# Optimization experiments

Hardware: AMD Instinct MI355X
Metric: run time of the kernel (lower is better)

Reference implementation:

```python
import jax, jax.numpy as jnp
import numpy as np

NEG_INF = -1e9

def setup_inputs() -> dict:
    key = jax.random.key(0)
    k1, k2, k3, k4, k5 = jax.random.split(key, 5)
    N, F_IN, F_OUT, H = 8192, 128, 32, 4
    node_features = jax.random.normal(k1, (N, F_IN), dtype=jnp.float32)
    adj_matrix = jax.random.randint(k2, (N, N), 0, 2, dtype=jnp.int32)
    # stacked per-head params (original: one Linear W [F_IN,F_OUT] + attention vec a [2*F_OUT] per head)
    W = jax.random.normal(k3, (H, F_IN, F_OUT), dtype=jnp.float32) * (1.0 / np.sqrt(F_IN))
    a_src = jax.random.normal(k4, (H, F_OUT), dtype=jnp.float32) * 0.1
    a_dst = jax.random.normal(k5, (H, F_OUT), dtype=jnp.float32) * 0.1
    return {"node_features": node_features, "adj_matrix": adj_matrix,
            "W": W, "a_src": a_src, "a_dst": a_dst}

def reference(node_features, adj_matrix, W, a_src, a_dst):
    alpha = 0.2  # LeakyReLU negative slope
    # project: [H, N, F_OUT]
    h = jnp.einsum('nf,hfo->hno', node_features, W)
    # GAT scores e_ij = LeakyReLU(a_src . h_i + a_dst . h_j), shape [H, N, N]
    e_src = jnp.einsum('hno,ho->hn', h, a_src)  # [H, N]
    e_dst = jnp.einsum('hno,ho->hn', h, a_dst)  # [H, N]
    e = jax.nn.leaky_relu(e_src[:, :, None] + e_dst[:, None, :], negative_slope=alpha)
    mask = (adj_matrix > 0)[None, :, :]
    attn = jax.nn.softmax(jnp.where(mask, e, NEG_INF), axis=-1)  # [H, N, N]
    out = jnp.einsum('hij,hjo->hio', attn, h)  # [H, N, F_OUT]
    # concat heads along feature dim -> [N, H*F_OUT]
    H_, N_, O_ = out.shape
    return jnp.transpose(out, (1, 0, 2)).reshape(N_, H_ * O_)
```

## Files before the change

### kernel.cpp

```cpp
#include <hip/hip_runtime.h>
#include <hip/hip_bf16.h>

#define NTOT 8192
#define FIN 128
#define FOUT 32
#define NH 4
#define NSEG 4
#define SEGJ (NTOT / NSEG)

typedef __attribute__((ext_vector_type(4))) float f32x4;
typedef __attribute__((ext_vector_type(4))) int i32x4;
typedef __attribute__((ext_vector_type(4))) unsigned int u32x4;
typedef __attribute__((ext_vector_type(8))) __bf16 bf16x8;
typedef unsigned long long u64;
typedef unsigned int u32;

__device__ __forceinline__ unsigned short f2bf(float x) {
  __hip_bfloat16 h = __float2bfloat16(x);
  return *reinterpret_cast<unsigned short*>(&h);
}

__global__ __launch_bounds__(256, 2) void k1_project(
    const float* __restrict__ X, const float* __restrict__ W,
    float* __restrict__ h, unsigned short* __restrict__ panel) {
  __shared__ float Xs[32 * 128];
  __shared__ float Ws[32 * 128];
  __shared__ unsigned short Hs[128 * 40];
  int t = threadIdx.x;
  int nb = blockIdx.x * 32;

  const f32x4* Xg = reinterpret_cast<const f32x4*>(X + (size_t)nb * FIN);
  f32x4* Xs4 = reinterpret_cast<f32x4*>(Xs);
#pragma unroll
  for (int r = 0; r < 4; ++r) Xs4[t + r * 256] = Xg[t + r * 256];

  int ng = t >> 5, oq = t & 31;
  int n0 = ng * 4, o0 = oq * 4;
  f32x4 acc[4];
#pragma unroll
  for (int nn = 0; nn < 4; ++nn) acc[nn] = (f32x4){0.f, 0.f, 0.f, 0.f};

  for (int kp = 0; kp < 4; ++kp) {
    __syncthreads();
#pragma unroll
    for (int r = 0; r < 4; ++r) {
      int q = t + r * 256;
      int flat = q * 4;
      int kk = flat >> 7;
      int c = flat & 127;
      int hdd = c >> 5;
      int oo = c & 31;
      *reinterpret_cast<f32x4*>(&Ws[kk * 128 + c]) =
          *reinterpret_cast<const f32x4*>(W + hdd * (FIN * FOUT) +
                                          (kp * 32 + kk) * FOUT + oo);
    }
    __syncthreads();
#pragma unroll 8
    for (int kk = 0; kk < 32; ++kk) {
      f32x4 wv = *reinterpret_cast<const f32x4*>(&Ws[kk * 128 + o0]);
#pragma unroll
      for (int nn = 0; nn < 4; ++nn)
        acc[nn] += Xs[(n0 + nn) * 128 + kp * 32 + kk] * wv;
    }
  }
#pragma unroll
  for (int nn = 0; nn < 4; ++nn) {
    *reinterpret_cast<f32x4*>(&h[(size_t)(nb + n0 + nn) * 128 + o0]) = acc[nn];
#pragma unroll
    for (int c = 0; c < 4; ++c)
      Hs[(o0 + c) * 40 + (n0 + nn)] = f2bf(acc[nn][c]);
  }
  __syncthreads();
  int jt = blockIdx.x;
#pragma unroll
  for (int it = 0; it < 2; ++it) {
    int item = t + it * 256;
    int p = item >> 6;
    int l = item & 63;
    int o = p * 16 + (l & 15);
    u32x4 v = *reinterpret_cast<const u32x4*>(&Hs[o * 40 + (l >> 4) * 8]);
    *reinterpret_cast<u32x4*>(panel + (size_t)(p * 256 + jt) * 512 + l * 8) = v;
  }
}

__global__ __launch_bounds__(256, 2) void k2_scores(
    const float* __restrict__ h, const float* __restrict__ a_src,
    const float* __restrict__ a_dst, float* __restrict__ Sf,
    float* __restrict__ E1f, float* __restrict__ E2f,
    unsigned short* __restrict__ Dbf, unsigned short* __restrict__ F1bf,
    unsigned short* __restrict__ F2bf) {
  int n = blockIdx.x * 256 + threadIdx.x;
  const f32x4* hv = reinterpret_cast<const f32x4*>(h + (size_t)n * 128);
  const f32x4* as4 = reinterpret_cast<const f32x4*>(a_src);
  const f32x4* ad4 = reinterpret_cast<const f32x4*>(a_dst);
  int jm = n >> 6, jo = n & 63;
#pragma unroll
  for (int hd = 0; hd < NH; ++hd) {
    f32x4 sa = {0.f, 0.f, 0.f, 0.f}, da = {0.f, 0.f, 0.f, 0.f};
#pragma unroll
    for (int q = 0; q < 8; ++q) {
      f32x4 x = hv[hd * 8 + q];
      sa += x * as4[hd * 8 + q];
      da += x * ad4[hd * 8 + q];
    }
    float s = (sa[0] + sa[1]) + (sa[2] + sa[3]);
    float d = (da[0] + da[1]) + (da[2] + da[3]);
    Sf[hd * NTOT + n] = s;
    E1f[hd * NTOT + n] = expf(s);
    E2f[hd * NTOT + n] = expf(0.2f * s);
    int ti = (jm * 4 + hd) * 64 + jo;
    Dbf[ti] = f2bf(d);
    F1bf[ti] = f2bf(expf(d));
    F2bf[ti] = f2bf(expf(0.2f * d));
  }
}

__global__ __launch_bounds__(256)
__attribute__((amdgpu_waves_per_eu(2))) void k3_attn(
    const int* __restrict__ adj, const float* __restrict__ Sf,
    const float* __restrict__ E1f, const float* __restrict__ E2f,
    const unsigned short* __restrict__ Dbf,
    const unsigned short* __restrict__ F1bf,
    const unsigned short* __restrict__ F2bf,
    const unsigned short* __restrict__ panel, float* __restrict__ pacc,
    float* __restrict__ plsum) {
  const int N = NTOT;
  int tid = threadIdx.x;
  int w = tid >> 6, l = tid & 63;
  int rh = w & 1, hp = w >> 1;
  int itile = blockIdx.x >> 2, seg = blockIdx.x & 3;
  int ibase = itile * 32 + rh * 16;
  int m = l & 15, g = l >> 4, jc = g * 8;
  int row = ibase + m;
  int hd0 = hp * 2;

  float sv0 = Sf[hd0 * N + row];
  float sv1 = Sf[(hd0 + 1) * N + row];

  const int* adjr = adj + (size_t)row * N + seg * SEGJ + jc;
  const char* dB =
      (const char*)Dbf + (size_t)(seg * 32) * 512 + hd0 * 128 + jc * 2;
  const char* f1B =
      (const char*)F1bf + (size_t)(seg * 32) * 512 + hd0 * 128 + jc * 2;
  const char* f2B =
      (const char*)F2bf + (size_t)(seg * 32) * 512 + hd0 * 128 + jc * 2;
  const char* pB = (const char*)panel +
                   ((size_t)(hd0 * 2) * 256 + seg * 64) * 1024 + (size_t)l * 16;
  const size_t PS = (size_t)256 * 1024;

  f32x4 z4 = {0.f, 0.f, 0.f, 0.f};
  f32x4 aP0[2] = {z4, z4}, aP1[2] = {z4, z4}, aPs[2] = {z4, z4};
  f32x4 aN0[2] = {z4, z4}, aN1[2] = {z4, z4}, aNs[2] = {z4, z4};
  bf16x8 bones;
  {
    u32 pat = (m == 0) ? 0x3f803f80u : 0u;
    u32x4 tmp = {pat, pat, pat, pat};
    bones = *reinterpret_cast<bf16x8*>(&tmp);
  }

#define MFM(AF, B, ACC) \
  ACC = __builtin_amdgcn_mfma_f32_16x16x32_bf16(AF, B, ACC, 0, 0, 0);

#define AFPLANE(HH, MK, Dv, F1v, F2v, B0, B1, SV)                         \
  {                                                                       \
    u32x4 aPw, aNw;                                                       \
    _Pragma("unroll") for (int p = 0; p < 4; ++p) {                       \
      float de = __uint_as_float(Dv[p] << 16);                            \
      float dodd = __uint_as_float(Dv[p] & 0xFFFF0000u);                  \
      u32 n0 = (u32)(__float_as_int((SV) + de) >> 31);                    \
      u32 n1 = (u32)(__float_as_int((SV) + dodd) >> 31);                  \
      u32 mn = __builtin_amdgcn_perm(n1, n0, 0x05040100u);                \
      aPw[p] = F1v[p] & ((MK)[p] & ~mn);                                  \
      aNw[p] = F2v[p] & ((MK)[p] & mn);                                   \
    }                                                                     \
    bf16x8 afP = *reinterpret_cast<bf16x8*>(&aPw);                        \
    bf16x8 afN = *reinterpret_cast<bf16x8*>(&aNw);                        \
    MFM(afP, B0, aP0[HH]) MFM(afP, B1, aP1[HH]) MFM(afP, bones, aPs[HH])  \
    MFM(afN, B0, aN0[HH]) MFM(afN, B1, aN1[HH]) MFM(afN, bones, aNs[HH])  \
  }

#pragma unroll 1
  for (int t = 0; t < 32; ++t) {
    const int* a_ = adjr + t * 64;
    i32x4 a0 = *reinterpret_cast<const i32x4*>(a_);
    i32x4 a1 = *reinterpret_cast<const i32x4*>(a_ + 4);
    i32x4 a2 = *reinterpret_cast<const i32x4*>(a_ + 32);
    i32x4 a3 = *reinterpret_cast<const i32x4*>(a_ + 36);
    u32x4 mkA, mkB;
#pragma unroll
    for (int p = 0; p < 2; ++p) {
      mkA[p] = __builtin_amdgcn_perm((u32)(-a0[2 * p + 1]), (u32)(-a0[2 * p]),
                                     0x05040100u);
      mkA[p + 2] = __builtin_amdgcn_perm((u32)(-a1[2 * p + 1]),
                                         (u32)(-a1[2 * p]), 0x05040100u);
      mkB[p] = __builtin_amdgcn_perm((u32)(-a2[2 * p + 1]), (u32)(-a2[2 * p]),
                                     0x05040100u);
      mkB[p + 2] = __builtin_amdgcn_perm((u32)(-a3[2 * p + 1]),
                                         (u32)(-a3[2 * p]), 0x05040100u);
    }
    size_t tb = (size_t)t * 512;
    size_t pb = (size_t)t * 2048;
#pragma unroll
    for (int hh = 0; hh < 2; ++hh) {
      float sv_ = hh ? sv1 : sv0;
      const char* d_ = dB + tb + hh * 128;
      const char* f1_ = f1B + tb + hh * 128;
      const char* f2_ = f2B + tb + hh * 128;
      const char* p0_ = pB + pb + (size_t)(hh * 2) * PS;
      const char* p1_ = p0_ + PS;
      {
        u32x4 Dv = *(const u32x4*)(d_);
        u32x4 F1v = *(const u32x4*)(f1_);
        u32x4 F2v = *(const u32x4*)(f2_);
        bf16x8 B0 = *(const bf16x8*)(p0_);
        bf16x8 B1 = *(const bf16x8*)(p1_);
        AFPLANE(hh, mkA, Dv, F1v, F2v, B0, B1, sv_)
      }
      {
        u32x4 Dv = *(const u32x4*)(d_ + 64);
        u32x4 F1v = *(const u32x4*)(f1_ + 64);
        u32x4 F2v = *(const u32x4*)(f2_ + 64);
        bf16x8 B0 = *(const bf16x8*)(p0_ + 1024);
        bf16x8 B1 = *(const bf16x8*)(p1_ + 1024);
        AFPLANE(hh, mkB, Dv, F1v, F2v, B0, B1, sv_)
      }
    }
  }
#undef AFPLANE
#undef MFM

#pragma unroll
  for (int hh = 0; hh < 2; ++hh) {
    int hd = hd0 + hh;
    int rb = ibase + g * 4;
#pragma unroll
    for (int r = 0; r < 4; ++r) {
      int rowr = rb + r;
      float e1 = E1f[hd * N + rowr], e2 = E2f[hd * N + rowr];
      if (m == 0)
        plsum[(seg * NH + hd) * N + rowr] =
            e1 * aPs[hh][r] + e2 * aNs[hh][r];
      pacc[((size_t)seg * N + rowr) * 128 + hd * 32 + m] =
          e1 * aP0[hh][r] + e2 * aN0[hh][r];
      pacc[((size_t)seg * N + rowr) * 128 + hd * 32 + 16 + m] =
          e1 * aP1[hh][r] + e2 * aN1[hh][r];
    }
  }
}

__global__ __launch_bounds__(256, 2) void k4_combine(
    const float* __restrict__ pacc, const float* __restrict__ plsum,
    float* __restrict__ out) {
  int idx = blockIdx.x * 256 + threadIdx.x;
  int i = idx >> 7;
  int c = idx & 127;
  int hd = c >> 5;
  float a = 0.f, ls = 0.f;
#pragma unroll
  for (int s = 0; s < NSEG; ++s) {
    a += pacc[((size_t)s * NTOT + i) * 128 + c];
    ls += plsum[(s * NH + hd) * NTOT + i];
  }
  out[idx] = (ls > 0.f) ? a / ls : 0.f;
}

extern "C" void kernel_launch(void* const* d_in, const int* in_sizes, int n_in,
                              void* d_out, int out_size, void* d_ws,
                              size_t ws_size, hipStream_t stream) {
  const float* X = (const float*)d_in[0];
  const int* adj = (const int*)d_in[1];
  const float* W = (const float*)d_in[2];
  const float* a_src = (const float*)d_in[3];
  const float* a_dst = (const float*)d_in[4];
  float* out = (float*)d_out;

  char* ws = (char*)d_ws;
  float* h = (float*)(ws + 0x0);
  unsigned short* panel = (unsigned short*)(ws + 0x400000);
  float* Sf = (float*)(ws + 0x600000);
  float* E1f = (float*)(ws + 0x620000);
  float* E2f = (float*)(ws + 0x640000);
  unsigned short* Dbf = (unsigned short*)(ws + 0x660000);
  unsigned short* F1bf = (unsigned short*)(ws + 0x670000);
  unsigned short* F2bf = (unsigned short*)(ws + 0x680000);
  float* pacc = (float*)(ws + 0x700000);
  float* plsum = (float*)(ws + 0x1700000);

  k1_project<<<dim3(256), dim3(256), 0, stream>>>(X, W, h, panel);
  k2_scores<<<dim3(32), dim3(256), 0, stream>>>(h, a_src, a_dst, Sf, E1f, E2f,
                                                Dbf, F1bf, F2bf);
  k3_attn<<<dim3(256 * NSEG), dim3(256), 0, stream>>>(
      adj, Sf, E1f, E2f, Dbf, F1bf, F2bf, panel, pacc, plsum);
  k4_combine<<<dim3(4096), dim3(256), 0, stream>>>(pacc, plsum, out);
}
```

Before: 170.4 us.

## Halve j-segments and software-pipeline adjacency loads with sched barriers

Reduces the column split from four to two segments, so each block processes 64 j-tiles and the grid halves. The attention loop is restructured so adjacency loads for tile t+2 are issued ahead in double-buffered registers, with sched_barrier fences fixing the order of loads and MFMA compute. The goal is to hide the latency of the large adjacency stream and cut partial-sum traffic in the combine step. In exchange there are fewer blocks for occupancy, higher register pressure, and a clamped redundant prefetch at the loop end.

```diff
diff --git a/kernel.cpp b/kernel.cpp
--- a/kernel.cpp
+++ b/kernel.cpp
@@ -5,7 +5,7 @@
 #define FIN 128
 #define FOUT 32
 #define NH 4
-#define NSEG 4
+#define NSEG 2
 #define SEGJ (NTOT / NSEG)
 
 typedef __attribute__((ext_vector_type(4))) float f32x4;
@@ -128,7 +128,7 @@
   int tid = threadIdx.x;
   int w = tid >> 6, l = tid & 63;
   int rh = w & 1, hp = w >> 1;
-  int itile = blockIdx.x >> 2, seg = blockIdx.x & 3;
+  int itile = blockIdx.x >> 1, seg = blockIdx.x & 1;
   int ibase = itile * 32 + rh * 16;
   int m = l & 15, g = l >> 4, jc = g * 8;
   int row = ibase + m;
@@ -139,13 +139,14 @@
 
   const int* adjr = adj + (size_t)row * N + seg * SEGJ + jc;
   const char* dB =
-      (const char*)Dbf + (size_t)(seg * 32) * 512 + hd0 * 128 + jc * 2;
+      (const char*)Dbf + (size_t)(seg * 64) * 512 + hd0 * 128 + jc * 2;
   const char* f1B =
-      (const char*)F1bf + (size_t)(seg * 32) * 512 + hd0 * 128 + jc * 2;
+      (const char*)F1bf + (size_t)(seg * 64) * 512 + hd0 * 128 + jc * 2;
   const char* f2B =
-      (const char*)F2bf + (size_t)(seg * 32) * 512 + hd0 * 128 + jc * 2;
+      (const char*)F2bf + (size_t)(seg * 64) * 512 + hd0 * 128 + jc * 2;
   const char* pB = (const char*)panel +
-                   ((size_t)(hd0 * 2) * 256 + seg * 64) * 1024 + (size_t)l * 16;
+                   ((size_t)(hd0 * 2) * 256 + seg * 128) * 1024 +
+                   (size_t)l * 16;
   const size_t PS = (size_t)256 * 1024;
 
   f32x4 z4 = {0.f, 0.f, 0.f, 0.f};
@@ -156,6 +157,71 @@
     u32 pat = (m == 0) ? 0x3f803f80u : 0u;
     u32x4 tmp = {pat, pat, pat, pat};
     bones = *reinterpret_cast<bf16x8*>(&tmp);
+  }
+
+  i32x4 Aa0, Aa1, Aa2, Aa3, Ba0, Ba1, Ba2, Ba3;
+  u32x4 D0a, D0b, D1a, D1b;
+  u32x4 F10a, F10b, F11a, F11b, F20a, F20b, F21a, F21b;
+  bf16x8 P00a, P00b, P01a, P01b, P10a, P10b, P11a, P11b;
+  u32x4 mkA, mkB;
+
+#define AISS(P, t_)                                            \
+  {                                                            \
+    int tc_ = (t_) > 63 ? 63 : (t_);                           \
+    const int* a_ = adjr + tc_ * 64;                           \
+    P##a0 = *reinterpret_cast<const i32x4*>(a_);               \
+    P##a1 = *reinterpret_cast<const i32x4*>(a_ + 4);           \
+    P##a2 = *reinterpret_cast<const i32x4*>(a_ + 32);          \
+    P##a3 = *reinterpret_cast<const i32x4*>(a_ + 36);          \
+  }                                                            \
+  __builtin_amdgcn_sched_barrier(0);
+
+#define TLOAD(t_)                                              \
+  {                                                            \
+    size_t tb_ = (size_t)(t_)*512;                             \
+    size_t pb_ = (size_t)(t_)*2048;                            \
+    D0a = *(const u32x4*)(dB + tb_);                           \
+    D0b = *(const u32x4*)(dB + tb_ + 64);                      \
+    D1a = *(const u32x4*)(dB + tb_ + 128);                     \
+    D1b = *(const u32x4*)(dB + tb_ + 192);                     \
+    F10a = *(const u32x4*)(f1B + tb_);                         \
+    F10b = *(const u32x4*)(f1B + tb_ + 64);                    \
+    F11a = *(const u32x4*)(f1B + tb_ + 128);                   \
+    F11b = *(const u32x4*)(f1B + tb_ + 192);                   \
+    F20a = *(const u32x4*)(f2B + tb_);                         \
+    F20b = *(const u32x4*)(f2B + tb_ + 64);                    \
+    F21a = *(const u32x4*)(f2B + tb_ + 128);                   \
+    F21b = *(const u32x4*)(f2B + tb_ + 192);                   \
+    const char* pp_ = pB + pb_;                                \
+    P00a = *(const bf16x8*)(pp_);                              \
+    P00b = *(const bf16x8*)(pp_ + 1024);                       \
+    P01a = *(const bf16x8*)(pp_ + PS);                         \
+    P01b = *(const bf16x8*)(pp_ + PS + 1024);                  \
+    P10a = *(const bf16x8*)(pp_ + 2 * PS);                     \
+    P10b = *(const bf16x8*)(pp_ + 2 * PS + 1024);              \
+    P11a = *(const bf16x8*)(pp_ + 3 * PS);                     \
+    P11b = *(const bf16x8*)(pp_ + 3 * PS + 1024);              \
+  }                                                            \
+  __builtin_amdgcn_sched_barrier(0);
+
+#define MASKS(P)                                                          \
+  {                                                                       \
+    mkA[0] = __builtin_amdgcn_perm((u32)(-P##a0[1]), (u32)(-P##a0[0]),    \
+                                   0x05040100u);                          \
+    mkA[1] = __builtin_amdgcn_perm((u32)(-P##a0[3]), (u32)(-P##a0[2]),    \
+                                   0x05040100u);                          \
+    mkA[2] = __builtin_amdgcn_perm((u32)(-P##a1[1]), (u32)(-P##a1[0]),    \
+                                   0x05040100u);                          \
+    mkA[3] = __builtin_amdgcn_perm((u32)(-P##a1[3]), (u32)(-P##a1[2]),    \
+                                   0x05040100u);                          \
+    mkB[0] = __builtin_amdgcn_perm((u32)(-P##a2[1]), (u32)(-P##a2[0]),    \
+                                   0x05040100u);                          \
+    mkB[1] = __builtin_amdgcn_perm((u32)(-P##a2[3]), (u32)(-P##a2[2]),    \
+                                   0x05040100u);                          \
+    mkB[2] = __builtin_amdgcn_perm((u32)(-P##a3[1]), (u32)(-P##a3[0]),    \
+                                   0x05040100u);                          \
+    mkB[3] = __builtin_amdgcn_perm((u32)(-P##a3[3]), (u32)(-P##a3[2]),    \
+                                   0x05040100u);                          \
   }
 
 #define MFM(AF, B, ACC) \
@@ -179,55 +245,31 @@
     MFM(afN, B0, aN0[HH]) MFM(afN, B1, aN1[HH]) MFM(afN, bones, aNs[HH])  \
   }
 
+#define COMPUTE                                            \
+  AFPLANE(0, mkA, D0a, F10a, F20a, P00a, P01a, sv0)        \
+  AFPLANE(0, mkB, D0b, F10b, F20b, P00b, P01b, sv0)        \
+  AFPLANE(1, mkA, D1a, F11a, F21a, P10a, P11a, sv1)        \
+  AFPLANE(1, mkB, D1b, F11b, F21b, P10b, P11b, sv1)
+
+  AISS(A, 0)
+  AISS(B, 1)
 #pragma unroll 1
-  for (int t = 0; t < 32; ++t) {
-    const int* a_ = adjr + t * 64;
-    i32x4 a0 = *reinterpret_cast<const i32x4*>(a_);
-    i32x4 a1 = *reinterpret_cast<const i32x4*>(a_ + 4);
-    i32x4 a2 = *reinterpret_cast<const i32x4*>(a_ + 32);
-    i32x4 a3 = *reinterpret_cast<const i32x4*>(a_ + 36);
-    u32x4 mkA, mkB;
-#pragma unroll
-    for (int p = 0; p < 2; ++p) {
-      mkA[p] = __builtin_amdgcn_perm((u32)(-a0[2 * p + 1]), (u32)(-a0[2 * p]),
-                                     0x05040100u);
-      mkA[p + 2] = __builtin_amdgcn_perm((u32)(-a1[2 * p + 1]),
-                                         (u32)(-a1[2 * p]), 0x05040100u);
-      mkB[p] = __builtin_amdgcn_perm((u32)(-a2[2 * p + 1]), (u32)(-a2[2 * p]),
-                                     0x05040100u);
-      mkB[p + 2] = __builtin_amdgcn_perm((u32)(-a3[2 * p + 1]),
-                                         (u32)(-a3[2 * p]), 0x05040100u);
-    }
-    size_t tb = (size_t)t * 512;
-    size_t pb = (size_t)t * 2048;
-#pragma unroll
-    for (int hh = 0; hh < 2; ++hh) {
-      float sv_ = hh ? sv1 : sv0;
-      const char* d_ = dB + tb + hh * 128;
-      const char* f1_ = f1B + tb + hh * 128;
-      const char* f2_ = f2B + tb + hh * 128;
-      const char* p0_ = pB + pb + (size_t)(hh * 2) * PS;
-      const char* p1_ = p0_ + PS;
-      {
-        u32x4 Dv = *(const u32x4*)(d_);
-        u32x4 F1v = *(const u32x4*)(f1_);
-        u32x4 F2v = *(const u32x4*)(f2_);
-        bf16x8 B0 = *(const bf16x8*)(p0_);
-        bf16x8 B1 = *(const bf16x8*)(p1_);
-        AFPLANE(hh, mkA, Dv, F1v, F2v, B0, B1, sv_)
-      }
-      {
-        u32x4 Dv = *(const u32x4*)(d_ + 64);
-        u32x4 F1v = *(const u32x4*)(f1_ + 64);
-        u32x4 F2v = *(const u32x4*)(f2_ + 64);
-        bf16x8 B0 = *(const bf16x8*)(p0_ + 1024);
-        bf16x8 B1 = *(const bf16x8*)(p1_ + 1024);
-        AFPLANE(hh, mkB, Dv, F1v, F2v, B0, B1, sv_)
-      }
-    }
-  }
+  for (int tt = 0; tt < 32; ++tt) {
+    TLOAD(2 * tt)
+    MASKS(A)
+    AISS(A, 2 * tt + 2)
+    COMPUTE
+    TLOAD(2 * tt + 1)
+    MASKS(B)
+    AISS(B, 2 * tt + 3)
+    COMPUTE
+  }
+#undef AISS
+#undef TLOAD
+#undef MASKS
+#undef MFM
 #undef AFPLANE
-#undef MFM
+#undef COMPUTE
 
 #pragma unroll
   for (int hh = 0; hh < 2; ++hh) {
@@ -238,8 +280,7 @@
       int rowr = rb + r;
       float e1 = E1f[hd * N + rowr], e2 = E2f[hd * N + rowr];
       if (m == 0)
-        plsum[(seg * NH + hd) * N + rowr] =
-            e1 * aPs[hh][r] + e2 * aNs[hh][r];
+        plsum[(seg * NH + hd) * N + rowr] = e1 * aPs[hh][r] + e2 * aNs[hh][r];
       pacc[((size_t)seg * N + rowr) * 128 + hd * 32 + m] =
           e1 * aP0[hh][r] + e2 * aN0[hh][r];
       pacc[((size_t)seg * N + rowr) * 128 + hd * 32 + 16 + m] =
```

Measured after the change: 171.3 us. Within noise of the previous version (+0.5%).

## Process two row groups per wave and stage column score vectors in LDS

Applied to the files above, without the earlier changes.

Each wave in the attention kernel now handles 32 rows (two 16-row groups) instead of 16, so every loaded panel B fragment and column-score vector feeds twice as many MFMAs. The per-segment D/F1/F2 bf16 tables are first copied into 48 KB of shared memory, and the inner loop reads them from there instead of from global memory. The grid is halved to match. In exchange, accumulator registers double (24 f32x4 per lane), which adds register pressure and may reduce occupancy, and the 48 KB LDS allocation per block also limits how many blocks fit on a CU.

```diff
diff --git a/kernel.cpp b/kernel.cpp
--- a/kernel.cpp
+++ b/kernel.cpp
@@ -125,32 +125,45 @@
     const unsigned short* __restrict__ panel, float* __restrict__ pacc,
     float* __restrict__ plsum) {
   const int N = NTOT;
+  __shared__ char lds[49152];
   int tid = threadIdx.x;
   int w = tid >> 6, l = tid & 63;
   int rh = w & 1, hp = w >> 1;
   int itile = blockIdx.x >> 2, seg = blockIdx.x & 3;
-  int ibase = itile * 32 + rh * 16;
+  int rowblock = itile * 64 + rh * 32;
   int m = l & 15, g = l >> 4, jc = g * 8;
-  int row = ibase + m;
   int hd0 = hp * 2;
 
-  float sv0 = Sf[hd0 * N + row];
-  float sv1 = Sf[(hd0 + 1) * N + row];
-
-  const int* adjr = adj + (size_t)row * N + seg * SEGJ + jc;
-  const char* dB =
-      (const char*)Dbf + (size_t)(seg * 32) * 512 + hd0 * 128 + jc * 2;
-  const char* f1B =
-      (const char*)F1bf + (size_t)(seg * 32) * 512 + hd0 * 128 + jc * 2;
-  const char* f2B =
-      (const char*)F2bf + (size_t)(seg * 32) * 512 + hd0 * 128 + jc * 2;
-  const char* pB = (const char*)panel +
-                   ((size_t)(hd0 * 2) * 256 + seg * 64) * 1024 + (size_t)l * 16;
-  const size_t PS = (size_t)256 * 1024;
+  {
+    const char* gD = (const char*)Dbf + (size_t)seg * 16384;
+    const char* gF1 = (const char*)F1bf + (size_t)seg * 16384;
+    const char* gF2 = (const char*)F2bf + (size_t)seg * 16384;
+#pragma unroll
+    for (int it = 0; it < 4; ++it) {
+      int off = it * 4096 + tid * 16;
+      *(u32x4*)&lds[off] = *(const u32x4*)(gD + off);
+      *(u32x4*)&lds[16384 + off] = *(const u32x4*)(gF1 + off);
+      *(u32x4*)&lds[32768 + off] = *(const u32x4*)(gF2 + off);
+    }
+  }
+  __syncthreads();
+
+  float sv[2][2];
+#pragma unroll
+  for (int hh = 0; hh < 2; ++hh)
+#pragma unroll
+    for (int rg = 0; rg < 2; ++rg)
+      sv[hh][rg] = Sf[(hd0 + hh) * N + rowblock + rg * 16 + m];
+
+  const int* adjr0 = adj + (size_t)(rowblock + m) * N + seg * SEGJ + jc;
+  const int* adjr1 = adjr0 + (size_t)16 * N;
+  const char* panB = (const char*)panel + (size_t)l * 16;
 
   f32x4 z4 = {0.f, 0.f, 0.f, 0.f};
-  f32x4 aP0[2] = {z4, z4}, aP1[2] = {z4, z4}, aPs[2] = {z4, z4};
-  f32x4 aN0[2] = {z4, z4}, aN1[2] = {z4, z4}, aNs[2] = {z4, z4};
+  f32x4 aP0[4] = {z4, z4, z4, z4}, aP1[4] = {z4, z4, z4, z4},
+        aPs[4] = {z4, z4, z4, z4};
+  f32x4 aN0[4] = {z4, z4, z4, z4}, aN1[4] = {z4, z4, z4, z4},
+        aNs[4] = {z4, z4, z4, z4};
   bf16x8 bones;
   {
     u32 pat = (m == 0) ? 0x3f803f80u : 0u;
@@ -161,68 +174,70 @@
 #define MFM(AF, B, ACC) \
   ACC = __builtin_amdgcn_mfma_f32_16x16x32_bf16(AF, B, ACC, 0, 0, 0);
 
-#define AFPLANE(HH, MK, Dv, F1v, F2v, B0, B1, SV)                         \
+#define AFPLANE(IX, MK, Dv, F1v, F2v, B0, B1, SV)                         \
   {                                                                       \
     u32x4 aPw, aNw;                                                       \
     _Pragma("unroll") for (int p = 0; p < 4; ++p) {                       \
-      float de = __uint_as_float(Dv[p] << 16);                            \
-      float dodd = __uint_as_float(Dv[p] & 0xFFFF0000u);                  \
+      float de = __uint_as_float((Dv)[p] << 16);                          \
+      float dodd = __uint_as_float((Dv)[p] & 0xFFFF0000u);                \
       u32 n0 = (u32)(__float_as_int((SV) + de) >> 31);                    \
       u32 n1 = (u32)(__float_as_int((SV) + dodd) >> 31);                  \
       u32 mn = __builtin_amdgcn_perm(n1, n0, 0x05040100u);                \
-      aPw[p] = F1v[p] & ((MK)[p] & ~mn);                                  \
-      aNw[p] = F2v[p] & ((MK)[p] & mn);                                   \
+      aPw[p] = (F1v)[p] & ((MK)[p] & ~mn);                                \
+      aNw[p] = (F2v)[p] & ((MK)[p] & mn);                                 \
     }                                                                     \
     bf16x8 afP = *reinterpret_cast<bf16x8*>(&aPw);                        \
     bf16x8 afN = *reinterpret_cast<bf16x8*>(&aNw);                        \
-    MFM(afP, B0, aP0[HH]) MFM(afP, B1, aP1[HH]) MFM(afP, bones, aPs[HH])  \
-    MFM(afN, B0, aN0[HH]) MFM(afN, B1, aN1[HH]) MFM(afN, bones, aNs[HH])  \
+    MFM(afP, B0, aP0[IX]) MFM(afP, B1, aP1[IX]) MFM(afP, bones, aPs[IX])  \
+    MFM(afN, B0, aN0[IX]) MFM(afN, B1, aN1[IX]) MFM(afN, bones, aNs[IX])  \
   }
 
 #pragma unroll 1
   for (int t = 0; t < 32; ++t) {
-    const int* a_ = adjr + t * 64;
-    i32x4 a0 = *reinterpret_cast<const i32x4*>(a_);
-    i32x4 a1 = *reinterpret_cast<const i32x4*>(a_ + 4);
-    i32x4 a2 = *reinterpret_cast<const i32x4*>(a_ + 32);
-    i32x4 a3 = *reinterpret_cast<const i32x4*>(a_ + 36);
-    u32x4 mkA, mkB;
-#pragma unroll
-    for (int p = 0; p < 2; ++p) {
-      mkA[p] = __builtin_amdgcn_perm((u32)(-a0[2 * p + 1]), (u32)(-a0[2 * p]),
-                                     0x05040100u);
-      mkA[p + 2] = __builtin_amdgcn_perm((u32)(-a1[2 * p + 1]),
-                                         (u32)(-a1[2 * p]), 0x05040100u);
-      mkB[p] = __builtin_amdgcn_perm((u32)(-a2[2 * p + 1]), (u32)(-a2[2 * p]),
-                                     0x05040100u);
-      mkB[p + 2] = __builtin_amdgcn_perm((u32)(-a3[2 * p + 1]),
-                                         (u32)(-a3[2 * p]), 0x05040100u);
-    }
-    size_t tb = (size_t)t * 512;
-    size_t pb = (size_t)t * 2048;
+    const int* a0_ = adjr0 + t * 64;
+    const int* a1_ = adjr1 + t * 64;
+    i32x4 r0A0 = *(const i32x4*)(a0_), r0A1 = *(const i32x4*)(a0_ + 4);
+    i32x4 r0B0 = *(const i32x4*)(a0_ + 32), r0B1 = *(const i32x4*)(a0_ + 36);
+    i32x4 r1A0 = *(const i32x4*)(a1_), r1A1 = *(const i32x4*)(a1_ + 4);
+    i32x4 r1B0 = *(const i32x4*)(a1_ + 32), r1B1 = *(const i32x4*)(a1_ + 36);
+    u32x4 mk[2][2];
+#define MKB(DST, A0, A1)                                                    \
+  DST[0] = __builtin_amdgcn_perm((u32)(-(A0)[1]), (u32)(-(A0)[0]),          \
+                                 0x05040100u);                              \
+  DST[1] = __builtin_amdgcn_perm((u32)(-(A0)[3]), (u32)(-(A0)[2]),          \
+                                 0x05040100u);                              \
+  DST[2] = __builtin_amdgcn_perm((u32)(-(A1)[1]), (u32)(-(A1)[0]),          \
+                                 0x05040100u);                              \
+  DST[3] = __builtin_amdgcn_perm((u32)(-(A1)[3]), (u32)(-(A1)[2]),          \
+                                 0x05040100u);
+    MKB(mk[0][0], r0A0, r0A1)
+    MKB(mk[0][1], r0B0, r0B1)
+    MKB(mk[1][0], r1A0, r1A1)
+    MKB(mk[1][1], r1B0, r1B1)
+#undef MKB
+
 #pragma unroll
     for (int hh = 0; hh < 2; ++hh) {
-      float sv_ = hh ? sv1 : sv0;
-      const char* d_ = dB + tb + hh * 128;
-      const char* f1_ = f1B + tb + hh * 128;
-      const char* f2_ = f2B + tb + hh * 128;
-      const char* p0_ = pB + pb + (size_t)(hh * 2) * PS;
-      const char* p1_ = p0_ + PS;
-      {
-        u32x4 Dv = *(const u32x4*)(d_);
-        u32x4 F1v = *(const u32x4*)(f1_);
-        u32x4 F2v = *(const u32x4*)(f2_);
-        bf16x8 B0 = *(const bf16x8*)(p0_);
-        bf16x8 B1 = *(const bf16x8*)(p1_);
-        AFPLANE(hh, mkA, Dv, F1v, F2v, B0, B1, sv_)
-      }
-      {
-        u32x4 Dv = *(const u32x4*)(d_ + 64);
-        u32x4 F1v = *(const u32x4*)(f1_ + 64);
-        u32x4 F2v = *(const u32x4*)(f2_ + 64);
-        bf16x8 B0 = *(const bf16x8*)(p0_ + 1024);
-        bf16x8 B1 = *(const bf16x8*)(p1_ + 1024);
-        AFPLANE(hh, mkB, Dv, F1v, F2v, B0, B1, sv_)
+      int hd = hd0 + hh;
+      int tb = t * 512 + hd * 128 + g * 16;
+      u32x4 DvA = *(const u32x4*)&lds[tb];
+      u32x4 DvB = *(const u32x4*)&lds[tb + 64];
+      u32x4 F1A = *(const u32x4*)&lds[16384 + tb];
+      u32x4 F1B = *(const u32x4*)&lds[16384 + tb + 64];
+      u32x4 F2A = *(const u32x4*)&lds[32768 + tb];
+      u32x4 F2B = *(const u32x4*)&lds[32768 + tb + 64];
+      size_t jtg = (size_t)(seg * 64 + t * 2);
+      const char* p0 = panB + ((size_t)(hd * 2) * 256 + jtg) * 1024;
+      const char* p1 = panB + ((size_t)(hd * 2 + 1) * 256 + jtg) * 1024;
+      bf16x8 B0A = *(const bf16x8*)(p0);
+      bf16x8 B0B = *(const bf16x8*)(p0 + 1024);
+      bf16x8 B1A = *(const bf16x8*)(p1);
+      bf16x8 B1B = *(const bf16x8*)(p1 + 1024);
+#pragma unroll
+      for (int rg = 0; rg < 2; ++rg) {
+        float sv_ = sv[hh][rg];
+        AFPLANE(hh * 2 + rg, mk[rg][0], DvA, F1A, F2A, B0A, B1A, sv_)
+        AFPLANE(hh * 2 + rg, mk[rg][1], DvB, F1B, F2B, B0B, B1B, sv_)
       }
     }
   }
@@ -231,19 +246,23 @@
 
 #pragma unroll
   for (int hh = 0; hh < 2; ++hh) {
-    int hd = hd0 + hh;
-    int rb = ibase + g * 4;
-#pragma unroll
-    for (int r = 0; r < 4; ++r) {
-      int rowr = rb + r;
-      float e1 = E1f[hd * N + rowr], e2 = E2f[hd * N + rowr];
-      if (m == 0)
-        plsum[(seg * NH + hd) * N + rowr] =
-            e1 * aPs[hh][r] + e2 * aNs[hh][r];
-      pacc[((size_t)seg * N + rowr) * 128 + hd * 32 + m] =
-          e1 * aP0[hh][r] + e2 * aN0[hh][r];
-      pacc[((size_t)seg * N + rowr) * 128 + hd * 32 + 16 + m] =
-          e1 * aP1[hh][r] + e2 * aN1[hh][r];
+#pragma unroll
+    for (int rg = 0; rg < 2; ++rg) {
+      int hd = hd0 + hh;
+      int ix = hh * 2 + rg;
+      int rb = rowblock + rg * 16 + g * 4;
+#pragma unroll
+      for (int r = 0; r < 4; ++r) {
+        int rowr = rb + r;
+        float e1 = E1f[hd * N + rowr], e2 = E2f[hd * N + rowr];
+        if (m == 0)
+          plsum[(seg * NH + hd) * N + rowr] =
+              e1 * aPs[ix][r] + e2 * aNs[ix][r];
+        pacc[((size_t)seg * N + rowr) * 128 + hd * 32 + m] =
+            e1 * aP0[ix][r] + e2 * aN0[ix][r];
+        pacc[((size_t)seg * N + rowr) * 128 + hd * 32 + 16 + m] =
+            e1 * aP1[ix][r] + e2 * aN1[ix][r];
+      }
     }
   }
 }
@@ -289,7 +308,7 @@
   k1_project<<<dim3(256), dim3(256), 0, stream>>>(X, W, h, panel);
   k2_scores<<<dim3(32), dim3(256), 0, stream>>>(h, a_src, a_dst, Sf, E1f, E2f,
                                                 Dbf, F1bf, F2bf);
-  k3_attn<<<dim3(256 * NSEG), dim3(256), 0, stream>>>(
+  k3_attn<<<dim3(128 * NSEG), dim3(256), 0, stream>>>(
       adj, Sf, E1f, E2f, Dbf, F1bf, F2bf, panel, pacc, plsum);
   k4_combine<<<dim3(4096), dim3(256), 0, stream>>>(pacc, plsum, out);
 }
```

Result: slower. 191.4 us (+12.3%).

## Prepack adjacency into bitmasks and stage panel/score tables through LDS via DMA

Applied to the files above, without the earlier changes.

A new pre-kernel compresses the int32 adjacency matrix into 64-bit ballot bitmasks stored transposed, so the attention kernel reads bits instead of full ints, and each adjacency row is then read from memory once rather than once per head pair. The score tables (D, exp(d), exp(0.2d)) are interleaved into one buffer. Panel and table tiles are double-buffered into shared memory with global_load_lds, and the grid is remapped so that each block covers 64 rows and one head pair. The cost is an extra full pass over the 256 MB adjacency in k0, plus per-iteration barriers in the main loop.

```diff
diff --git a/kernel.cpp b/kernel.cpp
--- a/kernel.cpp
+++ b/kernel.cpp
@@ -18,6 +18,26 @@
 __device__ __forceinline__ unsigned short f2bf(float x) {
   __hip_bfloat16 h = __float2bfloat16(x);
   return *reinterpret_cast<unsigned short*>(&h);
+}
+
+__device__ __forceinline__ void dma16(const void* g, void* l) {
+  __builtin_amdgcn_global_load_lds(
+      (const __attribute__((address_space(1))) void*)g,
+      (__attribute__((address_space(3))) void*)l, 16, 0, 0);
+}
+
+__global__ __launch_bounds__(256, 2) void k0_pack(
+    const int* __restrict__ adj, u64* __restrict__ bits64T) {
+  int row = blockIdx.x * 4 + (threadIdx.x >> 6);
+  int l = threadIdx.x & 63;
+  const int* ap = adj + (size_t)row * NTOT + l;
+  u64* bp = bits64T + row;
+#pragma unroll 4
+  for (int j64 = 0; j64 < NTOT / 64; ++j64) {
+    int v = ap[j64 * 64];
+    u64 mske = __ballot(v != 0);
+    if (l == 0) bp[(size_t)j64 * NTOT] = mske;
+  }
 }
 
 __global__ __launch_bounds__(256, 2) void k1_project(
@@ -87,8 +107,7 @@
     const float* __restrict__ h, const float* __restrict__ a_src,
     const float* __restrict__ a_dst, float* __restrict__ Sf,
     float* __restrict__ E1f, float* __restrict__ E2f,
-    unsigned short* __restrict__ Dbf, unsigned short* __restrict__ F1bf,
-    unsigned short* __restrict__ F2bf) {
+    unsigned short* __restrict__ Tt) {
   int n = blockIdx.x * 256 + threadIdx.x;
   const f32x4* hv = reinterpret_cast<const f32x4*>(h + (size_t)n * 128);
   const f32x4* as4 = reinterpret_cast<const f32x4*>(a_src);
@@ -108,45 +127,41 @@
     Sf[hd * NTOT + n] = s;
     E1f[hd * NTOT + n] = expf(s);
     E2f[hd * NTOT + n] = expf(0.2f * s);
-    int ti = (jm * 4 + hd) * 64 + jo;
-    Dbf[ti] = f2bf(d);
-    F1bf[ti] = f2bf(expf(d));
-    F2bf[ti] = f2bf(expf(0.2f * d));
+    int ti = jm * 1024 + hd * 192 + jo;
+    Tt[ti] = f2bf(d);
+    Tt[ti + 64] = f2bf(expf(d));
+    Tt[ti + 128] = f2bf(expf(0.2f * d));
   }
 }
 
 __global__ __launch_bounds__(256)
 __attribute__((amdgpu_waves_per_eu(2))) void k3_attn(
-    const int* __restrict__ adj, const float* __restrict__ Sf,
+    const u64* __restrict__ bits64T, const float* __restrict__ Sf,
     const float* __restrict__ E1f, const float* __restrict__ E2f,
-    const unsigned short* __restrict__ Dbf,
-    const unsigned short* __restrict__ F1bf,
-    const unsigned short* __restrict__ F2bf,
+    const unsigned short* __restrict__ Tt,
     const unsigned short* __restrict__ panel, float* __restrict__ pacc,
     float* __restrict__ plsum) {
   const int N = NTOT;
+  __shared__ char panelS[2][8192];
+  __shared__ char tabS[2][2048];
   int tid = threadIdx.x;
   int w = tid >> 6, l = tid & 63;
-  int rh = w & 1, hp = w >> 1;
-  int itile = blockIdx.x >> 2, seg = blockIdx.x & 3;
-  int ibase = itile * 32 + rh * 16;
+  int bx = blockIdx.x;
+  int itile = bx >> 3, hp = (bx >> 2) & 1, seg = bx & 3;
+  int ibase = itile * 64;
   int m = l & 15, g = l >> 4, jc = g * 8;
-  int row = ibase + m;
+  int rowbase = ibase + w * 16;
+  int row = rowbase + m;
   int hd0 = hp * 2;
+  int jm0 = seg * 32;
 
   float sv0 = Sf[hd0 * N + row];
   float sv1 = Sf[(hd0 + 1) * N + row];
 
-  const int* adjr = adj + (size_t)row * N + seg * SEGJ + jc;
-  const char* dB =
-      (const char*)Dbf + (size_t)(seg * 32) * 512 + hd0 * 128 + jc * 2;
-  const char* f1B =
-      (const char*)F1bf + (size_t)(seg * 32) * 512 + hd0 * 128 + jc * 2;
-  const char* f2B =
-      (const char*)F2bf + (size_t)(seg * 32) * 512 + hd0 * 128 + jc * 2;
-  const char* pB = (const char*)panel +
-                   ((size_t)(hd0 * 2) * 256 + seg * 64) * 1024 + (size_t)l * 16;
-  const size_t PS = (size_t)256 * 1024;
+  const char* pgW = (const char*)panel +
+                    ((size_t)(hp * 4 + w) * 256 + (size_t)seg * 64) * 1024;
+  const char* tg = (const char*)Tt + (size_t)jm0 * 2048;
+  const u64* bptr = bits64T + (size_t)jm0 * N + rowbase;
 
   f32x4 z4 = {0.f, 0.f, 0.f, 0.f};
   f32x4 aP0[2] = {z4, z4}, aP1[2] = {z4, z4}, aPs[2] = {z4, z4};
@@ -158,6 +173,27 @@
     bones = *reinterpret_cast<bf16x8*>(&tmp);
   }
 
+#define STAGE(t_)                                                       \
+  {                                                                     \
+    int tc_ = (t_) > 31 ? 31 : (t_);                                    \
+    char* pb_ = panelS[(t_)&1];                                         \
+    dma16(pgW + (size_t)tc_ * 2048 + l * 16, pb_ + w * 2048);           \
+    dma16(pgW + (size_t)tc_ * 2048 + 1024 + l * 16,                     \
+          pb_ + w * 2048 + 1024);                                       \
+    if (w == 0) {                                                       \
+      dma16(tg + (size_t)tc_ * 2048 + l * 16, tabS[(t_)&1]);            \
+      dma16(tg + (size_t)tc_ * 2048 + 1024 + l * 16,                    \
+            tabS[(t_)&1] + 1024);                                       \
+    }                                                                   \
+  }
+
+#define MKFB(MK, BY)                                                    \
+  _Pragma("unroll") for (int p = 0; p < 4; ++p) {                       \
+    u32 lo_ = (u32)(((int)((BY) << (31 - 2 * p))) >> 31);               \
+    u32 hi_ = (u32)(((int)((BY) << (30 - 2 * p))) >> 31);               \
+    MK[p] = __builtin_amdgcn_perm(hi_, lo_, 0x07060100u);               \
+  }
+
 #define MFM(AF, B, ACC) \
   ACC = __builtin_amdgcn_mfma_f32_16x16x32_bf16(AF, B, ACC, 0, 0, 0);
 
@@ -165,13 +201,13 @@
   {                                                                       \
     u32x4 aPw, aNw;                                                       \
     _Pragma("unroll") for (int p = 0; p < 4; ++p) {                       \
-      float de = __uint_as_float(Dv[p] << 16);                            \
-      float dodd = __uint_as_float(Dv[p] & 0xFFFF0000u);                  \
+      float de = __uint_as_float((Dv)[p] << 16);                          \
+      float dodd = __uint_as_float((Dv)[p] & 0xFFFF0000u);                \
       u32 n0 = (u32)(__float_as_int((SV) + de) >> 31);                    \
       u32 n1 = (u32)(__float_as_int((SV) + dodd) >> 31);                  \
       u32 mn = __builtin_amdgcn_perm(n1, n0, 0x05040100u);                \
-      aPw[p] = F1v[p] & ((MK)[p] & ~mn);                                  \
-      aNw[p] = F2v[p] & ((MK)[p] & mn);                                   \
+      aPw[p] = (F1v)[p] & ((MK)[p] & ~mn);                                \
+      aNw[p] = (F2v)[p] & ((MK)[p] & mn);                                 \
     }                                                                     \
     bf16x8 afP = *reinterpret_cast<bf16x8*>(&aPw);                        \
     bf16x8 afN = *reinterpret_cast<bf16x8*>(&aNw);                        \
@@ -179,67 +215,57 @@
     MFM(afN, B0, aN0[HH]) MFM(afN, B1, aN1[HH]) MFM(afN, bones, aNs[HH])  \
   }
 
+  STAGE(0)
+  __syncthreads();
+
 #pragma unroll 1
   for (int t = 0; t < 32; ++t) {
-    const int* a_ = adjr + t * 64;
-    i32x4 a0 = *reinterpret_cast<const i32x4*>(a_);
-    i32x4 a1 = *reinterpret_cast<const i32x4*>(a_ + 4);
-    i32x4 a2 = *reinterpret_cast<const i32x4*>(a_ + 32);
-    i32x4 a3 = *reinterpret_cast<const i32x4*>(a_ + 36);
+    int cur = t & 1;
+    STAGE(t + 1)
+    u64 M = bptr[(size_t)t * N + m];
+    u32 byA = ((u32)M >> jc) & 0xFFu;
+    u32 byB = ((u32)(M >> 32) >> jc) & 0xFFu;
     u32x4 mkA, mkB;
-#pragma unroll
-    for (int p = 0; p < 2; ++p) {
-      mkA[p] = __builtin_amdgcn_perm((u32)(-a0[2 * p + 1]), (u32)(-a0[2 * p]),
-                                     0x05040100u);
-      mkA[p + 2] = __builtin_amdgcn_perm((u32)(-a1[2 * p + 1]),
-                                         (u32)(-a1[2 * p]), 0x05040100u);
-      mkB[p] = __builtin_amdgcn_perm((u32)(-a2[2 * p + 1]), (u32)(-a2[2 * p]),
-                                     0x05040100u);
-      mkB[p + 2] = __builtin_amdgcn_perm((u32)(-a3[2 * p + 1]),
-                                         (u32)(-a3[2 * p]), 0x05040100u);
-    }
-    size_t tb = (size_t)t * 512;
-    size_t pb = (size_t)t * 2048;
+    MKFB(mkA, byA)
+    MKFB(mkB, byB)
+    const char* pb = panelS[cur];
+    const char* tb = tabS[cur];
 #pragma unroll
     for (int hh = 0; hh < 2; ++hh) {
+      int hdo = (hd0 + hh) * 384;
       float sv_ = hh ? sv1 : sv0;
-      const char* d_ = dB + tb + hh * 128;
-      const char* f1_ = f1B + tb + hh * 128;
-      const char* f2_ = f2B + tb + hh * 128;
-      const char* p0_ = pB + pb + (size_t)(hh * 2) * PS;
-      const char* p1_ = p0_ + PS;
-      {
-        u32x4 Dv = *(const u32x4*)(d_);
-        u32x4 F1v = *(const u32x4*)(f1_);
-        u32x4 F2v = *(const u32x4*)(f2_);
-        bf16x8 B0 = *(const bf16x8*)(p0_);
-        bf16x8 B1 = *(const bf16x8*)(p1_);
-        AFPLANE(hh, mkA, Dv, F1v, F2v, B0, B1, sv_)
-      }
-      {
-        u32x4 Dv = *(const u32x4*)(d_ + 64);
-        u32x4 F1v = *(const u32x4*)(f1_ + 64);
-        u32x4 F2v = *(const u32x4*)(f2_ + 64);
-        bf16x8 B0 = *(const bf16x8*)(p0_ + 1024);
-        bf16x8 B1 = *(const bf16x8*)(p1_ + 1024);
-        AFPLANE(hh, mkB, Dv, F1v, F2v, B0, B1, sv_)
-      }
-    }
-  }
+      u32x4 DvA = *(const u32x4*)(tb + hdo + jc * 2);
+      u32x4 DvB = *(const u32x4*)(tb + hdo + 64 + jc * 2);
+      u32x4 F1A = *(const u32x4*)(tb + hdo + 128 + jc * 2);
+      u32x4 F1B = *(const u32x4*)(tb + hdo + 192 + jc * 2);
+      u32x4 F2A = *(const u32x4*)(tb + hdo + 256 + jc * 2);
+      u32x4 F2B = *(const u32x4*)(tb + hdo + 320 + jc * 2);
+      const char* p0 = pb + (hh * 2) * 2048 + l * 16;
+      const char* p1 = pb + (hh * 2 + 1) * 2048 + l * 16;
+      bf16x8 B0A = *(const bf16x8*)(p0);
+      bf16x8 B0B = *(const bf16x8*)(p0 + 1024);
+      bf16x8 B1A = *(const bf16x8*)(p1);
+      bf16x8 B1B = *(const bf16x8*)(p1 + 1024);
+      AFPLANE(hh, mkA, DvA, F1A, F2A, B0A, B1A, sv_)
+      AFPLANE(hh, mkB, DvB, F1B, F2B, B0B, B1B, sv_)
+    }
+    __syncthreads();
+  }
+#undef STAGE
+#undef MKFB
+#undef MFM
 #undef AFPLANE
-#undef MFM
 
 #pragma unroll
   for (int hh = 0; hh < 2; ++hh) {
     int hd = hd0 + hh;
-    int rb = ibase + g * 4;
+    int rb = rowbase + g * 4;
 #pragma unroll
     for (int r = 0; r < 4; ++r) {
       int rowr = rb + r;
       float e1 = E1f[hd * N + rowr], e2 = E2f[hd * N + rowr];
       if (m == 0)
-        plsum[(seg * NH + hd) * N + rowr] =
-            e1 * aPs[hh][r] + e2 * aNs[hh][r];
+        plsum[(seg * NH + hd) * N + rowr] = e1 * aPs[hh][r] + e2 * aNs[hh][r];
       pacc[((size_t)seg * N + rowr) * 128 + hd * 32 + m] =
           e1 * aP0[hh][r] + e2 * aN0[hh][r];
       pacc[((size_t)seg * N + rowr) * 128 + hd * 32 + 16 + m] =
@@ -280,16 +306,16 @@
   float* Sf = (float*)(ws + 0x600000);
   float* E1f = (float*)(ws + 0x620000);
   float* E2f = (float*)(ws + 0x640000);
-  unsigned short* Dbf = (unsigned short*)(ws + 0x660000);
-  unsigned short* F1bf = (unsigned short*)(ws + 0x670000);
-  unsigned short* F2bf = (unsigned short*)(ws + 0x680000);
-  float* pacc = (float*)(ws + 0x700000);
-  float* plsum = (float*)(ws + 0x1700000);
-
+  unsigned short* Tt = (unsigned short*)(ws + 0x660000);
+  u64* bits64T = (u64*)(ws + 0x6A0000);
+  float* pacc = (float*)(ws + 0xEA0000);
+  float* plsum = (float*)(ws + 0x1EA0000);
+
+  k0_pack<<<dim3(2048), dim3(256), 0, stream>>>(adj, bits64T);
   k1_project<<<dim3(256), dim3(256), 0, stream>>>(X, W, h, panel);
   k2_scores<<<dim3(32), dim3(256), 0, stream>>>(h, a_src, a_dst, Sf, E1f, E2f,
-                                                Dbf, F1bf, F2bf);
-  k3_attn<<<dim3(256 * NSEG), dim3(256), 0, stream>>>(
-      adj, Sf, E1f, E2f, Dbf, F1bf, F2bf, panel, pacc, plsum);
+                                                Tt);
+  k3_attn<<<dim3(128 * 2 * NSEG), dim3(256), 0, stream>>>(
+      bits64T, Sf, E1f, E2f, Tt, panel, pacc, plsum);
   k4_combine<<<dim3(4096), dim3(256), 0, stream>>>(pacc, plsum, out);
 }
```

Result: no change. 172.7 us (+1.3%).
